# Optimization experiments

Measured on AMD Instinct MI355X. Metric: run time of the kernel, lower is better.

Reference implementation:

```python
import jax, jax.numpy as jnp
import numpy as np
from jax import lax

VOCAB = 32000
D_MODEL = 1024
N_LAYERS = 4
D_STATE = 8
D_CONV = 4
EXPAND = 2
D_INNER = EXPAND * D_MODEL          # 2048
DT_RANK = (D_MODEL + 15) // 16      # 64
B, L = 2, 1024


def setup_inputs() -> dict:
    key = jax.random.key(0)
    ks = jax.random.split(key, 20)
    s = 0.02
    inp = {
        "input_ids": jax.random.randint(ks[0], (B, L), 0, VOCAB, dtype=jnp.int32),
        "embed": jax.random.normal(ks[1], (VOCAB, D_MODEL), jnp.float32) * s,
        "in_proj_w": jax.random.normal(ks[2], (N_LAYERS, 2 * D_INNER, D_MODEL), jnp.float32) * s,
        "conv_w": jax.random.normal(ks[3], (N_LAYERS, D_INNER, 1, D_CONV), jnp.float32) * s,
        "conv_b": jnp.zeros((N_LAYERS, D_INNER), jnp.float32),
        "x_proj_w": jax.random.normal(ks[4], (N_LAYERS, DT_RANK + 2 * D_STATE, D_INNER), jnp.float32) * s,
        "dt_proj_w": jax.random.normal(ks[5], (N_LAYERS, D_INNER, DT_RANK), jnp.float32) * s,
        "dt_proj_b": jax.random.normal(ks[6], (N_LAYERS, D_INNER), jnp.float32) * 0.1,
        "A_log": jnp.broadcast_to(jnp.log(jnp.arange(1, D_STATE + 1, dtype=jnp.float32)),
                                  (N_LAYERS, D_INNER, D_STATE)) + 0.0,
        "D": jnp.ones((N_LAYERS, D_INNER), jnp.float32),
        "out_proj_w": jax.random.normal(ks[7], (N_LAYERS, D_MODEL, D_INNER), jnp.float32) * s,
        "ln_g": jnp.ones((N_LAYERS, D_MODEL), jnp.float32),
        "ln_b": jnp.zeros((N_LAYERS, D_MODEL), jnp.float32),
        "fn_g": jnp.ones((D_MODEL,), jnp.float32),
        "fn_b": jnp.zeros((D_MODEL,), jnp.float32),
        "fc_w": jax.random.normal(ks[8], (VOCAB, D_MODEL), jnp.float32) * s,
        "fc_b": jnp.zeros((VOCAB,), jnp.float32),
    }
    return inp


def layer_norm(x, g, b, eps=1e-5):
    mu = jnp.mean(x, -1, keepdims=True)
    var = jnp.var(x, -1, keepdims=True)
    return (x - mu) * lax.rsqrt(var + eps) * g + b


def silu(x):
    return x * jax.nn.sigmoid(x)


def selective_scan(deltaA, deltaBu, C):
    # deltaA, deltaBu: (b,l,d,n); C: (b,l,n) -> y: (b,l,d)
    def step(h, inp):
        dA, dBu, c = inp
        h = dA * h + dBu                       # (b,d,n)
        y = jnp.einsum('bdn,bn->bd', h, c)
        return h, y
    h0 = jnp.zeros(deltaA.shape[:1] + deltaA.shape[2:], deltaA.dtype)
    _, ys = lax.scan(step, h0, (deltaA.transpose(1, 0, 2, 3),
                                deltaBu.transpose(1, 0, 2, 3),
                                C.transpose(1, 0, 2)))
    return ys.transpose(1, 0, 2)


def mamba_block(x, in_proj_w, conv_w, conv_b, x_proj_w, dt_proj_w, dt_proj_b, A_log, D, out_proj_w):
    # x: (b,l,d_model)
    xz = jnp.einsum('bld,ed->ble', x, in_proj_w)          # (b,l,2*di)
    xc, z = jnp.split(xz, 2, axis=-1)
    # causal depthwise conv1d, kernel D_CONV
    xc_ncl = xc.transpose(0, 2, 1)                         # (b,di,l)
    xc_ncl = lax.conv_general_dilated(
        xc_ncl, conv_w, window_strides=(1,), padding=[(D_CONV - 1, 0)],
        feature_group_count=D_INNER, dimension_numbers=('NCH', 'OIH', 'NCH'))
    xc = silu(xc_ncl.transpose(0, 2, 1) + conv_b)          # (b,l,di)
    x_dbl = jnp.einsum('bld,ed->ble', xc, x_proj_w)        # (b,l,dt_rank+2n)
    dt, Bm, Cm = jnp.split(x_dbl, [DT_RANK, DT_RANK + D_STATE], axis=-1)
    dt = jax.nn.softplus(jnp.einsum('blr,dr->bld', dt, dt_proj_w) + dt_proj_b)  # (b,l,di)
    A = -jnp.exp(A_log)                                    # (di,n)
    deltaA = jnp.exp(dt[..., None] * A)                    # (b,l,di,n)
    deltaBu = dt[..., None] * Bm[:, :, None, :] * xc[..., None]
    y = selective_scan(deltaA, deltaBu, Cm)                # (b,l,di)
    y = y + xc * D
    y = y * silu(z)
    return jnp.einsum('ble,de->bld', y, out_proj_w)


def reference(input_ids, embed, in_proj_w, conv_w, conv_b, x_proj_w, dt_proj_w,
              dt_proj_b, A_log, D, out_proj_w, ln_g, ln_b, fn_g, fn_b, fc_w, fc_b):
    x = embed[input_ids]                                   # (b,l,d)
    for i in range(N_LAYERS):
        out = mamba_block(x, in_proj_w[i], conv_w[i], conv_b[i], x_proj_w[i],
                          dt_proj_w[i], dt_proj_b[i], A_log[i], D[i], out_proj_w[i])
        x = layer_norm(out + x, ln_g[i], ln_b[i])
    x = layer_norm(x, fn_g, fn_b)
    logits = jnp.einsum('bld,vd->blv', x, fc_w) + fc_b
    return logits
```

## Files before the change

kernel.cpp:

```cpp
#include <hip/hip_runtime.h>
#include <cstddef>
#include <cstdint>

#define D_MODEL 1024
#define D_INNER 2048
#define DT_RANK 64
#define D_STATE 8
#define NLAYERS 4
#define BATCH 2
#define SEQ 1024
#define M_ROWS (BATCH*SEQ)
#define VOCAB 32000
#define XPAD 128
#define NC 32
#define LC 32
#define XSK 16
#define OSK 2

typedef __attribute__((ext_vector_type(8))) short short8;
typedef __attribute__((ext_vector_type(4))) float f32x4;

#define GPTR(p) (const __attribute__((address_space(1))) void*)(p)
#define LPTR(p) (__attribute__((address_space(3))) void*)(p)

__device__ __forceinline__ float sigmoidf_(float x) { return 1.f / (1.f + __expf(-x)); }

__device__ __forceinline__ unsigned short f2bf(float f) {
    unsigned u = __float_as_uint(f);
    u += 0x7fffu + ((u >> 16) & 1u);
    return (unsigned short)(u >> 16);
}
__device__ __forceinline__ float bf2f(unsigned short u) {
    return __uint_as_float((unsigned)u << 16);
}

__global__ __launch_bounds__(256) void cast_kernel(const float* __restrict__ in,
                                                   unsigned short* __restrict__ out, int n4)
{
    int i = blockIdx.x * 256 + threadIdx.x;
    if (i >= n4) return;
    float4 v = ((const float4*)in)[i];
    ushort4 o;
    o.x = f2bf(v.x); o.y = f2bf(v.y); o.z = f2bf(v.z); o.w = f2bf(v.w);
    ((ushort4*)out)[i] = o;
}

__global__ __launch_bounds__(256) void cast_pad_xproj(const float* __restrict__ in,
                                                      unsigned short* __restrict__ out)
{
    int i = blockIdx.x * 256 + threadIdx.x;
    if (i >= NLAYERS * XPAD * D_INNER / 4) return;
    int col4 = i & (D_INNER / 4 - 1);
    int row = (i >> 9) & (XPAD - 1);
    int layer = i >> 16;
    ushort4 o = {0, 0, 0, 0};
    if (row < 80) {
        float4 v = ((const float4*)(in + ((size_t)layer * 80 + row) * D_INNER))[col4];
        o.x = f2bf(v.x); o.y = f2bf(v.y); o.z = f2bf(v.z); o.w = f2bf(v.w);
    }
    ((ushort4*)out)[i] = o;
}

__global__ __launch_bounds__(256) void gather_kernel(const int* __restrict__ ids,
                                                     const float* __restrict__ embed,
                                                     float* __restrict__ x,
                                                     unsigned short* __restrict__ xb)
{
    int m = blockIdx.x;
    int t = threadIdx.x;
    int id = ids[m];
    float4 v = ((const float4*)(embed + (size_t)id * D_MODEL))[t];
    ((float4*)(x + (size_t)m * D_MODEL))[t] = v;
    ushort4 o;
    o.x = f2bf(v.x); o.y = f2bf(v.y); o.z = f2bf(v.z); o.w = f2bf(v.w);
    ((ushort4*)(xb + (size_t)m * D_MODEL))[t] = o;
}

template<int EPI>
__global__ __launch_bounds__(256) void gemm_bf16_nt(const unsigned short* __restrict__ A, int lda,
                                                    const unsigned short* __restrict__ B, int ldb,
                                                    void* __restrict__ Cv, int ldc,
                                                    int K, const float* __restrict__ bias)
{
    __shared__ unsigned short As[2][128 * 32];
    __shared__ unsigned short Bs[2][128 * 32];
    const int tid = threadIdx.x;

    const int gm = gridDim.x;
    const int bid = blockIdx.y * gm + blockIdx.x;
    const int q = (gm * gridDim.y) >> 3;
    const int swz = (bid & 7) * q + (bid >> 3);
    const int bm = (swz % gm) * 128, bn = (swz / gm) * 128;

    const int wid = tid >> 6, lane = tid & 63;
    const int wm = (wid >> 1) * 64, wn = (wid & 1) * 64;
    const int lrow = lane & 15, lkg = lane >> 4;

    const int srow = tid >> 2;
    const int ksrc = ((tid & 3) ^ ((srow >> 1) & 3)) * 8;
    const size_t kz = (size_t)blockIdx.z * K;
    const unsigned short* Ag = A + (size_t)(bm + srow) * lda + kz + ksrc;
    const unsigned short* Bg = B + (size_t)(bn + srow) * ldb + kz + ksrc;
    const size_t r64a = (size_t)64 * lda;
    const size_t r64b = (size_t)64 * ldb;

#define STAGE(buf, koff)                                                                              \
    do {                                                                                              \
        __builtin_amdgcn_global_load_lds(GPTR(Ag + (koff)),        LPTR(&As[buf][tid * 8]), 16, 0, 0);\
        __builtin_amdgcn_global_load_lds(GPTR(Ag + r64a + (koff)), LPTR(&As[buf][2048 + tid * 8]), 16, 0, 0);\
        __builtin_amdgcn_global_load_lds(GPTR(Bg + (koff)),        LPTR(&Bs[buf][tid * 8]), 16, 0, 0);\
        __builtin_amdgcn_global_load_lds(GPTR(Bg + r64b + (koff)), LPTR(&Bs[buf][2048 + tid * 8]), 16, 0, 0);\
    } while (0)

    f32x4 acc[4][4];
    #pragma unroll
    for (int i = 0; i < 4; ++i)
        #pragma unroll
        for (int j = 0; j < 4; ++j)
            acc[i][j] = f32x4{0.f, 0.f, 0.f, 0.f};

    STAGE(0, 0);

    int cur = 0;
    for (int k0 = 0; k0 < K; k0 += 32) {
        if (k0 + 32 < K) {
            STAGE(cur ^ 1, k0 + 32);
            asm volatile("s_waitcnt vmcnt(4)" ::: "memory");
        } else {
            asm volatile("s_waitcnt vmcnt(0)" ::: "memory");
        }
        __builtin_amdgcn_s_barrier();
        __builtin_amdgcn_sched_barrier(0);

        short8 af[4], bf[4];
        #pragma unroll
        for (int i = 0; i < 4; ++i) {
            int ra = wm + 16 * i + lrow;
            int pa = lkg ^ ((ra >> 1) & 3);
            af[i] = *(const short8*)(&As[cur][ra * 32 + pa * 8]);
            int rb = wn + 16 * i + lrow;
            int pb = lkg ^ ((rb >> 1) & 3);
            bf[i] = *(const short8*)(&Bs[cur][rb * 32 + pb * 8]);
        }
        __builtin_amdgcn_s_setprio(1);
        #pragma unroll
        for (int i = 0; i < 4; ++i)
            #pragma unroll
            for (int j = 0; j < 4; ++j)
                acc[i][j] = __builtin_amdgcn_mfma_f32_16x16x32_bf16(af[i], bf[j], acc[i][j], 0, 0, 0);
        __builtin_amdgcn_s_setprio(0);

        __builtin_amdgcn_s_barrier();
        cur ^= 1;
    }
#undef STAGE

    const int crow = bm + wm + lkg * 4;
    const int ccol = bn + wn + lrow;
    #pragma unroll
    for (int i = 0; i < 4; ++i) {
        #pragma unroll
        for (int j = 0; j < 4; ++j) {
            float bv = (EPI == 2 || EPI == 3) ? bias[ccol + 16 * j] : 0.f;
            #pragma unroll
            for (int r = 0; r < 4; ++r) {
                float v = acc[i][j][r] + bv;
                size_t off = (size_t)(crow + 16 * i + r) * ldc + ccol + 16 * j;
                if (EPI == 0) {
                    ((float*)Cv)[(size_t)blockIdx.z * M_ROWS * ldc + off] = v;
                } else if (EPI == 2) {
                    ((float*)Cv)[off] = v;
                } else {
                    if (EPI == 3) v = (v > 20.f) ? v : log1pf(__expf(v));
                    ((unsigned short*)Cv)[off] = f2bf(v);
                }
            }
        }
    }
}

__device__ __forceinline__ void rd_a8(const unsigned short* S, int base, int lrow, int lkg, short8 a[4][2]) {
    #pragma unroll
    for (int i = 0; i < 4; ++i)
        #pragma unroll
        for (int kk = 0; kk < 2; ++kk) {
            int row = base + i * 16 + lrow;
            int p = (kk * 4 + lkg) ^ (lrow & 7);
            a[i][kk] = *(const short8*)(S + row * 64 + p * 8);
        }
}
__device__ __forceinline__ void rd_b4(const unsigned short* S, int base, int lrow, int lkg, short8 b[2][2]) {
    #pragma unroll
    for (int j = 0; j < 2; ++j)
        #pragma unroll
        for (int kk = 0; kk < 2; ++kk) {
            int row = base + j * 16 + lrow;
            int p = (kk * 4 + lkg) ^ (lrow & 7);
            b[j][kk] = *(const short8*)(S + row * 64 + p * 8);
        }
}

__global__ __launch_bounds__(512) void gemm_bf16_8ph(const unsigned short* __restrict__ A, int lda,
                                                     const unsigned short* __restrict__ B, int ldb,
                                                     float* __restrict__ C, int ldc,
                                                     int K, const float* __restrict__ bias)
{
    __shared__ unsigned short As[2][256 * 64];
    __shared__ unsigned short Bs[2][256 * 64];
    const int tid = threadIdx.x;

    const int gm = gridDim.x;
    const int bid = blockIdx.y * gm + blockIdx.x;
    const int q = (gm * gridDim.y) >> 3;
    const int swz = (bid & 7) * q + (bid >> 3);
    const int bm = (swz % gm) * 256, bn = (swz / gm) * 256;

    const int wid = tid >> 6, lane = tid & 63;
    const int wr = wid >> 2, wc = wid & 3;
    const int arow0 = wr * 128;
    const int b0r = wc * 32, b1r = 128 + wc * 32;
    const int lrow = lane & 15, lkg = lane >> 4;

    const int sg = tid >> 3, su = tid & 7;
    const int ksrc = (su ^ (sg & 7)) * 8;
    const unsigned short* Ag = A + (size_t)(bm + sg) * lda + ksrc;
    const unsigned short* Bg = B + (size_t)(bn + sg) * ldb + ksrc;

#define STG_A_H(buf, kt, h) do {                                                                   \
    __builtin_amdgcn_global_load_lds(GPTR(Ag + (size_t)(kt) * 64 + (size_t)((h) * 128) * lda),     \
                                     LPTR(&As[buf][(h) * 8192 + tid * 8]), 16, 0, 0);              \
    __builtin_amdgcn_global_load_lds(GPTR(Ag + (size_t)(kt) * 64 + (size_t)((h) * 128 + 64) * lda),\
                                     LPTR(&As[buf][(h) * 8192 + 4096 + tid * 8]), 16, 0, 0);       \
} while (0)
#define STG_B_H(buf, kt, h) do {                                                                   \
    __builtin_amdgcn_global_load_lds(GPTR(Bg + (size_t)(kt) * 64 + (size_t)((h) * 128) * ldb),     \
                                     LPTR(&Bs[buf][(h) * 8192 + tid * 8]), 16, 0, 0);              \
    __builtin_amdgcn_global_load_lds(GPTR(Bg + (size_t)(kt) * 64 + (size_t)((h) * 128 + 64) * ldb),\
                                     LPTR(&Bs[buf][(h) * 8192 + 4096 + tid * 8]), 16, 0, 0);       \
} while (0)
#define WAIT4() asm volatile("s_waitcnt vmcnt(4)" ::: "memory")
#define WAIT0() asm volatile("s_waitcnt vmcnt(0)" ::: "memory")
#define PBAR() __builtin_amdgcn_s_barrier()
#define SBAR() __builtin_amdgcn_sched_barrier(0)
#define MFMA_Q(QA, BH) do {                                                                        \
    __builtin_amdgcn_s_setprio(1);                                                                 \
    _Pragma("unroll") for (int i = 0; i < 4; ++i)                                                  \
    _Pragma("unroll") for (int j = 0; j < 2; ++j)                                                  \
    _Pragma("unroll") for (int kk = 0; kk < 2; ++kk)                                               \
        acc[(QA) * 4 + i][(BH) * 2 + j] =                                                          \
            __builtin_amdgcn_mfma_f32_16x16x32_bf16(a[i][kk], b[j][kk],                            \
                                                    acc[(QA) * 4 + i][(BH) * 2 + j], 0, 0, 0);     \
    __builtin_amdgcn_s_setprio(0);                                                                 \
} while (0)

    f32x4 acc[8][4];
    #pragma unroll
    for (int i = 0; i < 8; ++i)
        #pragma unroll
        for (int j = 0; j < 4; ++j)
            acc[i][j] = f32x4{0.f, 0.f, 0.f, 0.f};

    short8 a[4][2], b[2][2];
    const int NT = K >> 6;
    const int NI = NT >> 1;

    STG_A_H(0, 0, 0); STG_A_H(0, 0, 1); STG_B_H(0, 0, 0); STG_B_H(0, 0, 1);
    STG_A_H(1, 1, 0);
    asm volatile("s_waitcnt vmcnt(2)" ::: "memory");
    PBAR();

    for (int it = 0; it < NI; ++it) {
        const int T0 = 2 * it, T1 = 2 * it + 1;
        const bool more = (it + 1 < NI);

        STG_A_H(1, T1, 1);
        rd_a8(As[0], arow0, lrow, lkg, a);
        rd_b4(Bs[0], b0r, lrow, lkg, b);
        WAIT4(); PBAR(); SBAR();
        MFMA_Q(0, 0);
        PBAR();
        STG_B_H(1, T1, 0);
        rd_b4(Bs[0], b1r, lrow, lkg, b);
        WAIT4(); PBAR(); SBAR();
        MFMA_Q(0, 1);
        PBAR();
        STG_B_H(1, T1, 1);
        rd_a8(As[0], arow0 + 64, lrow, lkg, a);
        WAIT4(); PBAR(); SBAR();
        MFMA_Q(1, 1);
        PBAR();
        rd_b4(Bs[0], b0r, lrow, lkg, b);
        if (more) { STG_A_H(0, T0 + 2, 0); WAIT4(); } else { WAIT0(); }
        PBAR(); SBAR();
        MFMA_Q(1, 0);
        PBAR();
        if (more) STG_A_H(0, T0 + 2, 1);
        rd_a8(As[1], arow0, lrow, lkg, a);
        rd_b4(Bs[1], b0r, lrow, lkg, b);
        WAIT4(); PBAR(); SBAR();
        MFMA_Q(0, 0);
        PBAR();
        if (more) STG_B_H(0, T0 + 2, 0);
        rd_b4(Bs[1], b1r, lrow, lkg, b);
        WAIT4(); PBAR(); SBAR();
        MFMA_Q(0, 1);
        PBAR();
        if (more) STG_B_H(0, T0 + 2, 1);
        rd_a8(As[1], arow0 + 64, lrow, lkg, a);
        WAIT4(); PBAR(); SBAR();
        MFMA_Q(1, 1);
        PBAR();
        rd_b4(Bs[1], b0r, lrow, lkg, b);
        if (more) { STG_A_H(1, T1 + 2, 0); WAIT4(); } else { WAIT0(); }
        PBAR(); SBAR();
        MFMA_Q(1, 0);
        PBAR();
    }
#undef STG_A_H
#undef STG_B_H
#undef WAIT4
#undef WAIT0
#undef PBAR
#undef SBAR
#undef MFMA_Q

    const int crow = bm + arow0 + lkg * 4;
    #pragma unroll
    for (int i = 0; i < 8; ++i) {
        #pragma unroll
        for (int j = 0; j < 4; ++j) {
            int ccol = bn + (j >> 1) * 128 + wc * 32 + (j & 1) * 16 + lrow;
            float bv = bias[ccol];
            float* Cp = C + (size_t)(crow + 16 * i) * ldc + ccol;
            #pragma unroll
            for (int r = 0; r < 4; ++r)
                Cp[(size_t)r * ldc] = acc[i][j][r] + bv;
        }
    }
}

__global__ __launch_bounds__(256) void reduce_xdbl(const float* __restrict__ part,
                                                   float* __restrict__ xdbl,
                                                   unsigned short* __restrict__ xdbl_b)
{
    int i = blockIdx.x * 256 + threadIdx.x;
    float4 s = ((const float4*)part)[i];
    #pragma unroll
    for (int z = 1; z < XSK; ++z) {
        float4 v = ((const float4*)part)[(size_t)z * (M_ROWS * XPAD / 4) + i];
        s.x += v.x; s.y += v.y; s.z += v.z; s.w += v.w;
    }
    ((float4*)xdbl)[i] = s;
    ushort4 o;
    o.x = f2bf(s.x); o.y = f2bf(s.y); o.z = f2bf(s.z); o.w = f2bf(s.w);
    ((ushort4*)xdbl_b)[i] = o;
}

__global__ __launch_bounds__(256) void conv_silu_kernel(const unsigned short* __restrict__ xzb,
                                                        const float* __restrict__ cw,
                                                        const float* __restrict__ cb,
                                                        unsigned short* __restrict__ xcb)
{
    int idx = blockIdx.x * 256 + threadIdx.x;
    int d = idx & (D_INNER - 1);
    int m = idx >> 11;
    int l = m & (SEQ - 1);
    int b = m >> 10;
    float w0 = cw[d * 4 + 0], w1 = cw[d * 4 + 1], w2 = cw[d * 4 + 2], w3 = cw[d * 4 + 3];
    float s = cb[d];
    const unsigned short* base = xzb + ((size_t)b * SEQ) * (2 * D_INNER) + d;
    if (l - 3 >= 0) s += bf2f(base[(size_t)(l - 3) * (2 * D_INNER)]) * w0;
    if (l - 2 >= 0) s += bf2f(base[(size_t)(l - 2) * (2 * D_INNER)]) * w1;
    if (l - 1 >= 0) s += bf2f(base[(size_t)(l - 1) * (2 * D_INNER)]) * w2;
    s += bf2f(base[(size_t)l * (2 * D_INNER)]) * w3;
    float v = s * sigmoidf_(s);
    xcb[(size_t)m * D_INNER + d] = f2bf(v);
}

__global__ __launch_bounds__(256) void scan_partial(const unsigned short* __restrict__ dtb,
                                                    const float* __restrict__ xdbl,
                                                    const unsigned short* __restrict__ xcb,
                                                    const float* __restrict__ A_log,
                                                    float* __restrict__ H,
                                                    float* __restrict__ P)
{
    const int tid = threadIdx.x;
    const int b = blockIdx.x & 1;
    const int c = (blockIdx.x >> 1) & (NC - 1);
    const int d = ((blockIdx.x >> 6) << 8) + tid;

    __shared__ float Bsm[LC][8];
    {
        int r = tid >> 3, n = tid & 7;
        Bsm[r][n] = xdbl[(size_t)(b * SEQ + c * LC + r) * XPAD + DT_RANK + n];
    }
    __syncthreads();

    float An[8];
    #pragma unroll
    for (int n = 0; n < 8; ++n) An[n] = -__expf(A_log[d * 8 + n]);
    float h[8] = {0.f,0.f,0.f,0.f,0.f,0.f,0.f,0.f};
    float p[8] = {1.f,1.f,1.f,1.f,1.f,1.f,1.f,1.f};

    const unsigned short* dtp = dtb + (size_t)(b * SEQ + c * LC) * D_INNER + d;
    const unsigned short* xcp = xcb + (size_t)(b * SEQ + c * LC) * D_INNER + d;
    for (int l = 0; l < LC; ++l) {
        float dtv = bf2f(dtp[(size_t)l * D_INNER]);
        float ux  = dtv * bf2f(xcp[(size_t)l * D_INNER]);
        #pragma unroll
        for (int n = 0; n < 8; ++n) {
            float dA = __expf(dtv * An[n]);
            h[n] = dA * h[n] + Bsm[l][n] * ux;
            p[n] *= dA;
        }
    }
    size_t base = (size_t)((b * NC + c) * 8) * D_INNER + d;
    #pragma unroll
    for (int n = 0; n < 8; ++n) {
        H[base + (size_t)n * D_INNER] = h[n];
        P[base + (size_t)n * D_INNER] = p[n];
    }
}

__global__ __launch_bounds__(256) void scan_combine(const float* __restrict__ H,
                                                    float* __restrict__ P )
{
    int idx = blockIdx.x * 256 + threadIdx.x;
    int d = idx & (D_INNER - 1);
    int n = (idx >> 11) & 7;
    int b = idx >> 14;
    float hp = 0.f;
    for (int c = 0; c < NC; ++c) {
        size_t base = (size_t)((b * NC + c) * 8 + n) * D_INNER + d;
        float Pv = P[base], Hv = H[base];
        P[base] = hp;
        hp = Pv * hp + Hv;
    }
}

__global__ __launch_bounds__(256) void scan_final(const unsigned short* __restrict__ dtb,
                                                  const float* __restrict__ xdbl,
                                                  const unsigned short* __restrict__ xcb,
                                                  const unsigned short* __restrict__ xzb,
                                                  const float* __restrict__ A_log,
                                                  const float* __restrict__ Dp,
                                                  const float* __restrict__ h0,
                                                  unsigned short* __restrict__ yb)
{
    const int tid = threadIdx.x;
    const int b = blockIdx.x & 1;
    const int c = (blockIdx.x >> 1) & (NC - 1);
    const int d = ((blockIdx.x >> 6) << 8) + tid;

    __shared__ float Bsm[LC][8];
    __shared__ float Csm[LC][8];
    {
        int r = tid >> 3, n = tid & 7;
        size_t xrow = (size_t)(b * SEQ + c * LC + r) * XPAD;
        Bsm[r][n] = xdbl[xrow + DT_RANK + n];
        Csm[r][n] = xdbl[xrow + DT_RANK + 8 + n];
    }
    __syncthreads();

    float An[8], h[8];
    size_t base = (size_t)((b * NC + c) * 8) * D_INNER + d;
    #pragma unroll
    for (int n = 0; n < 8; ++n) {
        An[n] = -__expf(A_log[d * 8 + n]);
        h[n] = h0[base + (size_t)n * D_INNER];
    }
    const float Dv = Dp[d];

    const unsigned short* dtp = dtb + (size_t)(b * SEQ + c * LC) * D_INNER + d;
    const unsigned short* xcp = xcb + (size_t)(b * SEQ + c * LC) * D_INNER + d;
    const unsigned short* zp  = xzb + (size_t)(b * SEQ + c * LC) * (2 * D_INNER) + D_INNER + d;
    unsigned short* ybp = yb + (size_t)(b * SEQ + c * LC) * D_INNER + d;

    for (int l = 0; l < LC; ++l) {
        float dtv = bf2f(dtp[(size_t)l * D_INNER]);
        float xcv = bf2f(xcp[(size_t)l * D_INNER]);
        float zv  = bf2f(zp[(size_t)l * (2 * D_INNER)]);
        float ux = dtv * xcv;
        float acc = 0.f;
        #pragma unroll
        for (int n = 0; n < 8; ++n) {
            float dA = __expf(dtv * An[n]);
            h[n] = dA * h[n] + Bsm[l][n] * ux;
            acc += h[n] * Csm[l][n];
        }
        float yv = (acc + xcv * Dv) * (zv * sigmoidf_(zv));
        ybp[(size_t)l * D_INNER] = f2bf(yv);
    }
}

template<int NEXTRA>
__global__ __launch_bounds__(256) void ln_kernel(const float* __restrict__ e0,
                                                 const float* __restrict__ e1,
                                                 const float* __restrict__ xin,
                                                 float* __restrict__ xout,
                                                 unsigned short* __restrict__ xbout,
                                                 const float* __restrict__ g,
                                                 const float* __restrict__ bb)
{
    int m = blockIdx.x;
    int t = threadIdx.x;
    float4 v = ((const float4*)(xin + (size_t)m * D_MODEL))[t];
    if (NEXTRA >= 1) {
        float4 e = ((const float4*)(e0 + (size_t)m * D_MODEL))[t];
        v.x += e.x; v.y += e.y; v.z += e.z; v.w += e.w;
    }
    if (NEXTRA >= 2) {
        float4 e = ((const float4*)(e1 + (size_t)m * D_MODEL))[t];
        v.x += e.x; v.y += e.y; v.z += e.z; v.w += e.w;
    }
    float s  = v.x + v.y + v.z + v.w;
    float s2 = v.x * v.x + v.y * v.y + v.z * v.z + v.w * v.w;
    for (int off = 32; off; off >>= 1) {
        s  += __shfl_down(s, off);
        s2 += __shfl_down(s2, off);
    }
    __shared__ float red[8];
    int wid = t >> 6, lane = t & 63;
    if (lane == 0) { red[wid] = s; red[wid + 4] = s2; }
    __syncthreads();
    if (t == 0) {
        float a  = red[0] + red[1] + red[2] + red[3];
        float b2 = red[4] + red[5] + red[6] + red[7];
        float mu = a * (1.f / D_MODEL);
        red[0] = mu;
        red[4] = b2 * (1.f / D_MODEL) - mu * mu;
    }
    __syncthreads();
    float mu = red[0];
    float rs = rsqrtf(red[4] + 1e-5f);
    float4 gg = ((const float4*)g)[t];
    float4 bv = ((const float4*)bb)[t];
    float4 o;
    o.x = (v.x - mu) * rs * gg.x + bv.x;
    o.y = (v.y - mu) * rs * gg.y + bv.y;
    o.z = (v.z - mu) * rs * gg.z + bv.z;
    o.w = (v.w - mu) * rs * gg.w + bv.w;
    ((float4*)(xout + (size_t)m * D_MODEL))[t] = o;
    ushort4 ob;
    ob.x = f2bf(o.x); ob.y = f2bf(o.y); ob.z = f2bf(o.z); ob.w = f2bf(o.w);
    ((ushort4*)(xbout + (size_t)m * D_MODEL))[t] = ob;
}

extern "C" void kernel_launch(void* const* d_in, const int* in_sizes, int n_in,
                              void* d_out, int out_size, void* d_ws, size_t ws_size,
                              hipStream_t stream)
{
    const int*   ids      = (const int*)d_in[0];
    const float* embed    = (const float*)d_in[1];
    const float* in_proj  = (const float*)d_in[2];
    const float* conv_w   = (const float*)d_in[3];
    const float* conv_b   = (const float*)d_in[4];
    const float* x_proj   = (const float*)d_in[5];
    const float* dt_w     = (const float*)d_in[6];
    const float* dt_b     = (const float*)d_in[7];
    const float* A_log    = (const float*)d_in[8];
    const float* Dp       = (const float*)d_in[9];
    const float* out_proj = (const float*)d_in[10];
    const float* ln_g     = (const float*)d_in[11];
    const float* ln_b     = (const float*)d_in[12];
    const float* fn_g     = (const float*)d_in[13];
    const float* fn_b     = (const float*)d_in[14];
    const float* fc_w     = (const float*)d_in[15];
    const float* fc_b     = (const float*)d_in[16];
    float* logits = (float*)d_out;

    float* ws = (float*)d_ws;
    float* x     = ws;
    float* xdbl  = x + (size_t)M_ROWS * D_MODEL;
    float* tmp   = xdbl + (size_t)M_ROWS * XPAD;
    float* xpart = tmp + (size_t)M_ROWS * D_MODEL;

    float* Hbuf = tmp;
    float* Pbuf = tmp + (size_t)BATCH * NC * D_STATE * D_INNER;
    float* opart = xpart;

    unsigned short* xb     = (unsigned short*)(xpart + (size_t)XSK * M_ROWS * XPAD);
    unsigned short* yb     = xb + (size_t)M_ROWS * D_MODEL;
    unsigned short* xzb    = yb + (size_t)M_ROWS * D_INNER;
    unsigned short* xcb    = xzb + (size_t)M_ROWS * 2 * D_INNER;
    unsigned short* dtb    = xcb + (size_t)M_ROWS * D_INNER;
    unsigned short* xdbl_b = dtb + (size_t)M_ROWS * D_INNER;
    unsigned short* wb_in  = xdbl_b + (size_t)M_ROWS * XPAD;
    unsigned short* wb_out = wb_in + (size_t)NLAYERS * 2 * D_INNER * D_MODEL;
    unsigned short* wb_fc  = wb_out + (size_t)NLAYERS * D_MODEL * D_INNER;
    unsigned short* wb_x   = wb_fc + (size_t)VOCAB * D_MODEL;
    unsigned short* wb_dt  = wb_x + (size_t)NLAYERS * XPAD * D_INNER;

    {
        int n4 = NLAYERS * 2 * D_INNER * D_MODEL / 4;
        cast_kernel<<<(n4 + 255) / 256, 256, 0, stream>>>(in_proj, wb_in, n4);
        n4 = NLAYERS * D_MODEL * D_INNER / 4;
        cast_kernel<<<(n4 + 255) / 256, 256, 0, stream>>>(out_proj, wb_out, n4);
        n4 = VOCAB * D_MODEL / 4;
        cast_kernel<<<(n4 + 255) / 256, 256, 0, stream>>>(fc_w, wb_fc, n4);
        n4 = NLAYERS * D_INNER * DT_RANK / 4;
        cast_kernel<<<(n4 + 255) / 256, 256, 0, stream>>>(dt_w, wb_dt, n4);
        n4 = NLAYERS * XPAD * D_INNER / 4;
        cast_pad_xproj<<<(n4 + 255) / 256, 256, 0, stream>>>(x_proj, wb_x);
    }

    gather_kernel<<<M_ROWS, 256, 0, stream>>>(ids, embed, x, xb);

    for (int i = 0; i < NLAYERS; ++i) {
        const unsigned short* W_in_b  = wb_in + (size_t)i * 2 * D_INNER * D_MODEL;
        const unsigned short* W_out_b = wb_out + (size_t)i * D_MODEL * D_INNER;
        const unsigned short* W_x_b   = wb_x + (size_t)i * XPAD * D_INNER;
        const unsigned short* W_dt_b  = wb_dt + (size_t)i * D_INNER * DT_RANK;
        const float* cw    = conv_w + (size_t)i * D_INNER * 4;
        const float* cb    = conv_b + (size_t)i * D_INNER;
        const float* b_dt  = dt_b + (size_t)i * D_INNER;
        const float* Al    = A_log + (size_t)i * D_INNER * D_STATE;
        const float* Dl    = Dp + (size_t)i * D_INNER;
        const float* g     = ln_g + (size_t)i * D_MODEL;
        const float* bb    = ln_b + (size_t)i * D_MODEL;

        gemm_bf16_nt<1><<<dim3(M_ROWS / 128, 2 * D_INNER / 128), 256, 0, stream>>>(
            xb, D_MODEL, W_in_b, D_MODEL, xzb, 2 * D_INNER, D_MODEL, nullptr);

        conv_silu_kernel<<<(M_ROWS * D_INNER) / 256, 256, 0, stream>>>(xzb, cw, cb, xcb);

        gemm_bf16_nt<0><<<dim3(M_ROWS / 128, 1, XSK), 256, 0, stream>>>(
            xcb, D_INNER, W_x_b, D_INNER, xpart, XPAD, D_INNER / XSK, nullptr);
        reduce_xdbl<<<(M_ROWS * XPAD / 4) / 256, 256, 0, stream>>>(xpart, xdbl, xdbl_b);

        gemm_bf16_nt<3><<<dim3(M_ROWS / 128, D_INNER / 128), 256, 0, stream>>>(
            xdbl_b, XPAD, W_dt_b, DT_RANK, dtb, D_INNER, DT_RANK, b_dt);

        scan_partial<<<BATCH * NC * (D_INNER / 256), 256, 0, stream>>>(
            dtb, xdbl, xcb, Al, Hbuf, Pbuf);
        scan_combine<<<(BATCH * D_STATE * D_INNER) / 256, 256, 0, stream>>>(Hbuf, Pbuf);
        scan_final<<<BATCH * NC * (D_INNER / 256), 256, 0, stream>>>(
            dtb, xdbl, xcb, xzb, Al, Dl, Pbuf, yb);

        gemm_bf16_nt<0><<<dim3(M_ROWS / 128, D_MODEL / 128, OSK), 256, 0, stream>>>(
            yb, D_INNER, W_out_b, D_INNER, opart, D_MODEL, D_INNER / OSK, nullptr);

        ln_kernel<2><<<M_ROWS, 256, 0, stream>>>(
            opart, opart + (size_t)M_ROWS * D_MODEL, x, x, xb, g, bb);
    }

    ln_kernel<0><<<M_ROWS, 256, 0, stream>>>(nullptr, nullptr, x, tmp, xb, fn_g, fn_b);

    gemm_bf16_8ph<<<dim3(M_ROWS / 256, VOCAB / 256), 512, 0, stream>>>(
        xb, D_MODEL, wb_fc, D_MODEL, logits, VOCAB, D_MODEL, fc_b);
}
```

Measured before the change: 899.1 us.

## Rework GEMM LDS prefetch schedule to full-tile lookahead and reuse B fragment

Restructures the double-buffered global-to-LDS pipeline in the 256x256 bf16 GEMM so both k-tiles are fully staged before the loop. Most per-quarter vmcnt waits are dropped; only one wait remains per half-iteration. A separate b0s register set holds the first B fragment, so the fourth MFMA quarter reuses it instead of re-reading it from LDS. This removes redundant LDS reads and wait stalls at the cost of extra VGPRs and more in-flight loads, which could reduce occupancy or introduce hazards if the wait counts are wrong.

```diff
diff --git a/kernel.cpp b/kernel.cpp
--- a/kernel.cpp
+++ b/kernel.cpp
@@ -238,17 +238,16 @@
     __builtin_amdgcn_global_load_lds(GPTR(Bg + (size_t)(kt) * 64 + (size_t)((h) * 128 + 64) * ldb),\
                                      LPTR(&Bs[buf][(h) * 8192 + 4096 + tid * 8]), 16, 0, 0);       \
 } while (0)
-#define WAIT4() asm volatile("s_waitcnt vmcnt(4)" ::: "memory")
-#define WAIT0() asm volatile("s_waitcnt vmcnt(0)" ::: "memory")
+#define WAITN(n) asm volatile("s_waitcnt vmcnt(" #n ")" ::: "memory")
 #define PBAR() __builtin_amdgcn_s_barrier()
 #define SBAR() __builtin_amdgcn_sched_barrier(0)
-#define MFMA_Q(QA, BH) do {                                                                        \
+#define MFMA_Q(QA, BH, BARR) do {                                                                  \
     __builtin_amdgcn_s_setprio(1);                                                                 \
     _Pragma("unroll") for (int i = 0; i < 4; ++i)                                                  \
     _Pragma("unroll") for (int j = 0; j < 2; ++j)                                                  \
     _Pragma("unroll") for (int kk = 0; kk < 2; ++kk)                                               \
         acc[(QA) * 4 + i][(BH) * 2 + j] =                                                          \
-            __builtin_amdgcn_mfma_f32_16x16x32_bf16(a[i][kk], b[j][kk],                            \
+            __builtin_amdgcn_mfma_f32_16x16x32_bf16(a[i][kk], BARR[j][kk],                         \
                                                     acc[(QA) * 4 + i][(BH) * 2 + j], 0, 0, 0);     \
     __builtin_amdgcn_s_setprio(0);                                                                 \
 } while (0)
@@ -260,66 +259,65 @@
         for (int j = 0; j < 4; ++j)
             acc[i][j] = f32x4{0.f, 0.f, 0.f, 0.f};
 
-    short8 a[4][2], b[2][2];
+    short8 a[4][2], b[2][2], b0s[2][2];
     const int NT = K >> 6;
     const int NI = NT >> 1;
 
     STG_A_H(0, 0, 0); STG_A_H(0, 0, 1); STG_B_H(0, 0, 0); STG_B_H(0, 0, 1);
-    STG_A_H(1, 1, 0);
-    asm volatile("s_waitcnt vmcnt(2)" ::: "memory");
+    STG_A_H(1, 1, 0); STG_A_H(1, 1, 1); STG_B_H(1, 1, 0); STG_B_H(1, 1, 1);
+    WAITN(8);
     PBAR();
 
     for (int it = 0; it < NI; ++it) {
-        const int T0 = 2 * it, T1 = 2 * it + 1;
+        const int T0n = 2 * it + 2, T1n = 2 * it + 3;
         const bool more = (it + 1 < NI);
 
-        STG_A_H(1, T1, 1);
         rd_a8(As[0], arow0, lrow, lkg, a);
-        rd_b4(Bs[0], b0r, lrow, lkg, b);
-        WAIT4(); PBAR(); SBAR();
-        MFMA_Q(0, 0);
-        PBAR();
-        STG_B_H(1, T1, 0);
+        rd_b4(Bs[0], b0r, lrow, lkg, b0s);
+        PBAR(); SBAR();
+        MFMA_Q(0, 0, b0s);
+        PBAR();
         rd_b4(Bs[0], b1r, lrow, lkg, b);
-        WAIT4(); PBAR(); SBAR();
-        MFMA_Q(0, 1);
-        PBAR();
-        STG_B_H(1, T1, 1);
+        PBAR(); SBAR();
+        MFMA_Q(0, 1, b);
+        PBAR();
+        if (more) STG_B_H(0, T0n, 0);
         rd_a8(As[0], arow0 + 64, lrow, lkg, a);
-        WAIT4(); PBAR(); SBAR();
-        MFMA_Q(1, 1);
-        PBAR();
-        rd_b4(Bs[0], b0r, lrow, lkg, b);
-        if (more) { STG_A_H(0, T0 + 2, 0); WAIT4(); } else { WAIT0(); }
-        PBAR(); SBAR();
-        MFMA_Q(1, 0);
-        PBAR();
-        if (more) STG_A_H(0, T0 + 2, 1);
+        PBAR(); SBAR();
+        MFMA_Q(1, 1, b);
+        PBAR();
+        if (more) { STG_A_H(0, T0n, 0); WAITN(4); } else { WAITN(0); }
+        PBAR(); SBAR();
+        MFMA_Q(1, 0, b0s);
+        PBAR();
+        if (more) { STG_A_H(0, T0n, 1); STG_B_H(0, T0n, 1); }
         rd_a8(As[1], arow0, lrow, lkg, a);
-        rd_b4(Bs[1], b0r, lrow, lkg, b);
-        WAIT4(); PBAR(); SBAR();
-        MFMA_Q(0, 0);
-        PBAR();
-        if (more) STG_B_H(0, T0 + 2, 0);
+        rd_b4(Bs[1], b0r, lrow, lkg, b0s);
+        PBAR(); SBAR();
+        MFMA_Q(0, 0, b0s);
+        PBAR();
         rd_b4(Bs[1], b1r, lrow, lkg, b);
-        WAIT4(); PBAR(); SBAR();
-        MFMA_Q(0, 1);
-        PBAR();
-        if (more) STG_B_H(0, T0 + 2, 1);
+        PBAR(); SBAR();
+        MFMA_Q(0, 1, b);
+        PBAR();
+        if (more) STG_B_H(1, T1n, 0);
         rd_a8(As[1], arow0 + 64, lrow, lkg, a);
-        WAIT4(); PBAR(); SBAR();
-        MFMA_Q(1, 1);
-        PBAR();
-        rd_b4(Bs[1], b0r, lrow, lkg, b);
-        if (more) { STG_A_H(1, T1 + 2, 0); WAIT4(); } else { WAIT0(); }
-        PBAR(); SBAR();
-        MFMA_Q(1, 0);
+        PBAR(); SBAR();
+        MFMA_Q(1, 1, b);
+        PBAR();
+        if (more) {
+            STG_B_H(1, T1n, 1); STG_A_H(1, T1n, 0); STG_A_H(1, T1n, 1);
+            WAITN(8);
+        } else {
+            WAITN(0);
+        }
+        PBAR(); SBAR();
+        MFMA_Q(1, 0, b0s);
         PBAR();
     }
 #undef STG_A_H
 #undef STG_B_H
-#undef WAIT4
-#undef WAIT0
+#undef WAITN
 #undef PBAR
 #undef SBAR
 #undef MFMA_Q
```

Result: no change. 893.5 us (-0.6%).
